# Kernel tuning notes

Hardware: AMD Instinct MI355X
Metric: run time of the kernel (lower is better)

## Reference

```python
import jax, jax.numpy as jnp
import numpy as np

E = 16           # num_experts
D = 4096         # hidden_size
F = 688          # per-expert SwiGLU intermediate size
N = 8192         # total tokens (bsz*seq_len)
CAP_FACTOR = 1.25


def setup_inputs() -> dict:
    key = jax.random.key(0)
    k1, k2, k3, k4, k5, k6 = jax.random.split(key, 6)
    return {
        "x": jax.random.normal(k1, (N, D), dtype=jnp.float32),
        "topk_idx": jax.random.randint(k2, (N,), 0, E, dtype=jnp.int32),
        "topk_scores": jax.random.uniform(k3, (N,), dtype=jnp.float32),
        "Wg": jax.random.normal(k4, (E, D, F), dtype=jnp.float32) * 0.02,
        "Wu": jax.random.normal(k5, (E, D, F), dtype=jnp.float32) * 0.02,
        "Wd": jax.random.normal(k6, (E, F, D), dtype=jnp.float32) * 0.02,
    }


def reference(x, topk_idx, topk_scores, Wg, Wu, Wd):
    # Switch-style top-1 MoE with capacity-based token dropping.
    # Deterministic variant: tokens beyond capacity are dropped in token order
    # (original uses randperm; the math pattern is identical).
    n, d = x.shape
    e = Wg.shape[0]
    cap = int(CAP_FACTOR * n / e)  # static under jit

    # position of each token within its assigned expert (0-based)
    oh = jax.nn.one_hot(topk_idx, e, dtype=jnp.int32)            # [N, E]
    pos = jnp.take_along_axis(jnp.cumsum(oh, axis=0) - 1,
                              topk_idx[:, None].astype(jnp.int32), axis=1)[:, 0]
    keep = pos < cap                                             # [N] bool

    # dispatch: scatter kept tokens into [E, cap, D]; dropped go to dummy row E
    e_safe = jnp.where(keep, topk_idx, e)
    p_safe = jnp.minimum(pos, cap - 1)
    buf = jnp.zeros((e + 1, cap, d), x.dtype).at[e_safe, p_safe].set(x)[:e]

    # per-expert SwiGLU FFN: down(silu(gate(x)) * up(x))
    h = jax.nn.silu(jnp.einsum('ecd,edf->ecf', buf, Wg)) \
        * jnp.einsum('ecd,edf->ecf', buf, Wu)                    # [E, cap, F]
    out = jnp.einsum('ecf,efd->ecd', h, Wd)                      # [E, cap, D]

    # combine: gather back, zero-pad dropped tokens, scale by gate scores
    y = out[topk_idx, p_safe] * keep[:, None].astype(x.dtype)
    y = y * topk_scores[:, None]
    return y
```

## Files before the change

### kernel.cpp

```cpp
#include <hip/hip_runtime.h>
#include <hip/hip_bf16.h>

#define E_ 16
#define D_ 4096
#define F_ 688
#define N_ 8192
#define CAP_ 640
#define NKT_ 64
#define NFT_ 11

typedef __attribute__((ext_vector_type(8))) short bf16x8;
typedef __attribute__((ext_vector_type(4))) float f32x4;
typedef __attribute__((ext_vector_type(4))) float fvec4;
typedef __attribute__((ext_vector_type(8))) unsigned short usvec8;

__device__ __forceinline__ unsigned short f2bf(float f) {
    __hip_bfloat16 h = __float2bfloat16(f);
    return __builtin_bit_cast(unsigned short, h);
}
__device__ __forceinline__ int lidx(int row, int k) {
    return row * 64 + (((k >> 3) ^ (row & 7)) << 3) + (k & 7);
}
__device__ __forceinline__ int bidx(int row, int k) {
    return row * 64 + (((k >> 3) ^ ((row >> 1) & 7)) << 3) + (k & 7);
}
__device__ __forceinline__ void gload16(const unsigned short* g, unsigned short* l) {
    __builtin_amdgcn_global_load_lds(
        (const __attribute__((address_space(1))) unsigned int*)g,
        (__attribute__((address_space(3))) unsigned int*)l, 16, 0, 0);
}

__global__ void k_dispatch(const int* __restrict__ idx,
                           int* __restrict__ slot_token,
                           int* __restrict__ row_of,
                           int* __restrict__ cnt) {
    __shared__ int hist[256][E_];
    const int t = threadIdx.x;
#pragma unroll
    for (int e = 0; e < E_; e++) hist[t][e] = 0;
    __syncthreads();
    const int base = t * (N_ / 256);
    for (int j = 0; j < N_ / 256; j++) {
        int e = idx[base + j];
        hist[t][e]++;
    }
    __syncthreads();
    if (t < E_) {
        int run = 0;
        for (int i = 0; i < 256; i++) { int v = hist[i][t]; hist[i][t] = run; run += v; }
        cnt[t] = run < CAP_ ? run : CAP_;
    }
    for (int s = t; s < E_ * CAP_; s += 256) slot_token[s] = -1;
    __syncthreads();
    for (int j = 0; j < N_ / 256; j++) {
        int i = base + j;
        int e = idx[i];
        int p = hist[t][e]++;
        if (p < CAP_) { slot_token[e * CAP_ + p] = i; row_of[i] = e * CAP_ + p; }
        else          { row_of[i] = -1; }
    }
}

__global__ void k_zero_dropped(const int* __restrict__ row_of, float* __restrict__ y) {
    const int i = blockIdx.x;
    if (row_of[i] >= 0) return;
    fvec4* yp = (fvec4*)(y + (size_t)i * D_);
    fvec4 z = {0.f, 0.f, 0.f, 0.f};
    for (int c = threadIdx.x; c < D_ / 4; c += 256) yp[c] = z;
}

__global__ void k_gather(const float* __restrict__ x, const int* __restrict__ slot_token,
                         unsigned short* __restrict__ Aimg) {
    const int strip = blockIdx.y;
    const int kg = blockIdx.x;
    const int t = threadIdx.x;
    const int r = t >> 1, h = t & 1;
    const int tok = slot_token[strip * 128 + r];
#pragma unroll
    for (int kl4 = 0; kl4 < 4; kl4++) {
        const int kt = kg * 4 + kl4;
        const int k0 = kt * 64 + h * 32;
        unsigned short* dst = Aimg + ((size_t)strip * NKT_ + kt) * 8192;
        usvec8 p[4];
        if (tok < 0) {
            usvec8 z = {0, 0, 0, 0, 0, 0, 0, 0};
            p[0] = z; p[1] = z; p[2] = z; p[3] = z;
        } else {
            const float* src = x + (size_t)tok * D_ + k0;
#pragma unroll
            for (int uu = 0; uu < 4; uu++) {
                fvec4 a = *(const fvec4*)(src + uu * 8);
                fvec4 b = *(const fvec4*)(src + uu * 8 + 4);
                usvec8 q = {f2bf(a[0]), f2bf(a[1]), f2bf(a[2]), f2bf(a[3]),
                            f2bf(b[0]), f2bf(b[1]), f2bf(b[2]), f2bf(b[3])};
                p[uu] = q;
            }
        }
#pragma unroll
        for (int uu = 0; uu < 4; uu++)
            *(usvec8*)&dst[lidx(r, h * 32 + uu * 8)] = p[uu];
    }
}

__global__ __launch_bounds__(256, 2) void k_gemm1(
    const unsigned short* __restrict__ Aimg,
    const float* __restrict__ Wg, const float* __restrict__ Wu,
    const int* __restrict__ cnt, unsigned short* __restrict__ Himg) {
    const int bid = blockIdx.x;
    const int xcd = bid & 7;
    const int j = bid >> 3;
    const int mb = j % 5;
    const int gl = j / 5;
    const int group = xcd * 22 + gl;
    const int e = group / NFT_, fidx = group % NFT_;
    const int m0 = mb * 128, f0 = fidx * 64;
    if (m0 >= cnt[e]) return;
    const int strip = e * 5 + mb;

    __shared__ __align__(16) unsigned short As[2][128 * 64];
    __shared__ __align__(16) unsigned short Bgs[2][64 * 64];
    __shared__ __align__(16) unsigned short Bus[2][64 * 64];

    const int tid = threadIdx.x;
    const int lane = tid & 63, wave = tid >> 6;
    const int wm = wave >> 1, wn = wave & 1;

    f32x4 accG[4][2], accU[4][2];
#pragma unroll
    for (int a = 0; a < 4; a++)
#pragma unroll
        for (int b = 0; b < 2; b++) {
            f32x4 z = {0.f, 0.f, 0.f, 0.f};
            accG[a][b] = z; accU[a][b] = z;
        }

    const int fpos = (tid & 31) * 2, kq8 = (tid >> 5) * 8;
    const int gf = f0 + fpos;
    const bool bvalid = gf < F_;
    const float2 fz2 = {0.f, 0.f};
    const float* WgE = Wg + (size_t)e * D_ * F_;
    const float* WuE = Wu + (size_t)e * D_ * F_;
    const unsigned short* Astrip = Aimg + (size_t)strip * NKT_ * 8192;

    {
#pragma unroll
        for (int i = 0; i < 4; i++) {
            int off = (wave * 4 + i) * 512;
            gload16(Astrip + off + lane * 8, &As[0][off]);
        }
        float2 g[8], u[8];
#pragma unroll
        for (int r = 0; r < 8; r++) {
            size_t off = (size_t)(kq8 + r) * F_ + gf;
            g[r] = bvalid ? *(const float2*)(WgE + off) : fz2;
            u[r] = bvalid ? *(const float2*)(WuE + off) : fz2;
        }
        usvec8 pg0, pg1, pu0, pu1;
#pragma unroll
        for (int r = 0; r < 8; r++) {
            pg0[r] = (short)f2bf(g[r].x); pg1[r] = (short)f2bf(g[r].y);
            pu0[r] = (short)f2bf(u[r].x); pu1[r] = (short)f2bf(u[r].y);
        }
        *(usvec8*)&Bgs[0][bidx(fpos, kq8)]     = pg0;
        *(usvec8*)&Bgs[0][bidx(fpos + 1, kq8)] = pg1;
        *(usvec8*)&Bus[0][bidx(fpos, kq8)]     = pu0;
        *(usvec8*)&Bus[0][bidx(fpos + 1, kq8)] = pu1;
    }
    __syncthreads();

    for (int kt = 0; kt < NKT_; ++kt) {
        const int cur = kt & 1, nxt = cur ^ 1;
        const bool hn = (kt + 1 < NKT_);
        float2 g[8], u[8];
        if (hn) {
            const unsigned short* asrc = Astrip + (size_t)(kt + 1) * 8192;
#pragma unroll
            for (int i = 0; i < 4; i++) {
                int off = (wave * 4 + i) * 512;
                gload16(asrc + off + lane * 8, &As[nxt][off]);
            }
#pragma unroll
            for (int r = 0; r < 8; r++) {
                size_t off = ((size_t)(kt + 1) * 64 + kq8 + r) * F_ + gf;
                g[r] = bvalid ? *(const float2*)(WgE + off) : fz2;
                u[r] = bvalid ? *(const float2*)(WuE + off) : fz2;
            }
        }
        __builtin_amdgcn_s_setprio(1);
#pragma unroll
        for (int kk = 0; kk < 64; kk += 32) {
            const int ko = kk + ((lane >> 4) << 3);
            bf16x8 av[4], bgv[2], buv[2];
#pragma unroll
            for (int mi = 0; mi < 4; mi++)
                av[mi] = *(const bf16x8*)&As[cur][lidx(wm * 64 + mi * 16 + (lane & 15), ko)];
#pragma unroll
            for (int ni = 0; ni < 2; ni++) {
                int rr = wn * 32 + ni * 16 + (lane & 15);
                bgv[ni] = *(const bf16x8*)&Bgs[cur][bidx(rr, ko)];
                buv[ni] = *(const bf16x8*)&Bus[cur][bidx(rr, ko)];
            }
#pragma unroll
            for (int mi = 0; mi < 4; mi++)
#pragma unroll
                for (int ni = 0; ni < 2; ni++) {
                    accG[mi][ni] = __builtin_amdgcn_mfma_f32_16x16x32_bf16(av[mi], bgv[ni], accG[mi][ni], 0, 0, 0);
                    accU[mi][ni] = __builtin_amdgcn_mfma_f32_16x16x32_bf16(av[mi], buv[ni], accU[mi][ni], 0, 0, 0);
                }
        }
        __builtin_amdgcn_s_setprio(0);
        if (hn) {
            usvec8 pg0, pg1, pu0, pu1;
#pragma unroll
            for (int r = 0; r < 8; r++) {
                pg0[r] = (short)f2bf(g[r].x); pg1[r] = (short)f2bf(g[r].y);
                pu0[r] = (short)f2bf(u[r].x); pu1[r] = (short)f2bf(u[r].y);
            }
            *(usvec8*)&Bgs[nxt][bidx(fpos, kq8)]     = pg0;
            *(usvec8*)&Bgs[nxt][bidx(fpos + 1, kq8)] = pg1;
            *(usvec8*)&Bus[nxt][bidx(fpos, kq8)]     = pu0;
            *(usvec8*)&Bus[nxt][bidx(fpos + 1, kq8)] = pu1;
        }
        __syncthreads();
    }

    unsigned short* Ht = Himg + ((size_t)strip * NFT_ + fidx) * 8192;
#pragma unroll
    for (int mi = 0; mi < 4; mi++)
#pragma unroll
        for (int ni = 0; ni < 2; ni++) {
            int fl = wn * 32 + ni * 16 + (lane & 15);
            int rl = wm * 64 + mi * 16 + ((lane >> 4) << 2);
#pragma unroll
            for (int q = 0; q < 4; q++) {
                float g = accG[mi][ni][q], u = accU[mi][ni][q];
                float h = g * u / (1.f + __expf(-g));
                Ht[lidx(rl + q, fl)] = f2bf(h);
            }
        }
}

__global__ __launch_bounds__(256, 3) void k_gemm2(
    const unsigned short* __restrict__ Himg, const float* __restrict__ Wd,
    const int* __restrict__ slot_token, const int* __restrict__ cnt,
    const float* __restrict__ scores, float* __restrict__ y) {
    const int bid = blockIdx.x;
    const int xcd = bid & 7;
    const int j = bid >> 3;
    const int mb = j % 5;
    const int gl = j / 5;
    const int group = xcd * 128 + gl;
    const int e = group >> 6, didx = group & 63;
    const int m0 = mb * 128, d0 = didx * 64;
    if (m0 >= cnt[e]) return;
    const int strip = e * 5 + mb;

    __shared__ __align__(16) unsigned short As[2][128 * 64];
    __shared__ __align__(16) unsigned short Bts[2][64 * 64];
    __shared__ int tokS[128];
    __shared__ float scS[128];

    const int tid = threadIdx.x;
    const int lane = tid & 63, wave = tid >> 6;
    const int wm = wave >> 1, wn = wave & 1;

    if (tid < 128) {
        int t = slot_token[e * CAP_ + m0 + tid];
        tokS[tid] = t;
        scS[tid] = (t >= 0) ? scores[t] : 0.f;
    }

    f32x4 acc[4][2];
#pragma unroll
    for (int a = 0; a < 4; a++)
#pragma unroll
        for (int b = 0; b < 2; b++) {
            f32x4 z = {0.f, 0.f, 0.f, 0.f};
            acc[a][b] = z;
        }

    const int dpos = (tid & 31) * 2, kq8 = (tid >> 5) * 8;
    const int gd = d0 + dpos;
    const float2 fz2 = {0.f, 0.f};
    const float* WdE = Wd + (size_t)e * F_ * D_;
    const unsigned short* Hstrip = Himg + (size_t)strip * NFT_ * 8192;

    {
#pragma unroll
        for (int i = 0; i < 4; i++) {
            int off = (wave * 4 + i) * 512;
            gload16(Hstrip + off + lane * 8, &As[0][off]);
        }
        float2 b[8];
#pragma unroll
        for (int r = 0; r < 8; r++) {
            int kr = kq8 + r;
            b[r] = (kr < F_) ? *(const float2*)(WdE + (size_t)kr * D_ + gd) : fz2;
        }
        usvec8 p0, p1;
#pragma unroll
        for (int r = 0; r < 8; r++) { p0[r] = (short)f2bf(b[r].x); p1[r] = (short)f2bf(b[r].y); }
        *(usvec8*)&Bts[0][bidx(dpos, kq8)]     = p0;
        *(usvec8*)&Bts[0][bidx(dpos + 1, kq8)] = p1;
    }
    __syncthreads();

    for (int fc = 0; fc < NFT_; ++fc) {
        const int cur = fc & 1, nxt = cur ^ 1;
        const bool hn = (fc + 1 < NFT_);
        float2 b[8];
        if (hn) {
            const unsigned short* asrc = Hstrip + (size_t)(fc + 1) * 8192;
#pragma unroll
            for (int i = 0; i < 4; i++) {
                int off = (wave * 4 + i) * 512;
                gload16(asrc + off + lane * 8, &As[nxt][off]);
            }
#pragma unroll
            for (int r = 0; r < 8; r++) {
                int kr = (fc + 1) * 64 + kq8 + r;
                b[r] = (kr < F_) ? *(const float2*)(WdE + (size_t)kr * D_ + gd) : fz2;
            }
        }
        __builtin_amdgcn_s_setprio(1);
#pragma unroll
        for (int kk = 0; kk < 64; kk += 32) {
            const int ko = kk + ((lane >> 4) << 3);
            bf16x8 av[4], bv[2];
#pragma unroll
            for (int mi = 0; mi < 4; mi++)
                av[mi] = *(const bf16x8*)&As[cur][lidx(wm * 64 + mi * 16 + (lane & 15), ko)];
#pragma unroll
            for (int ni = 0; ni < 2; ni++)
                bv[ni] = *(const bf16x8*)&Bts[cur][bidx(wn * 32 + ni * 16 + (lane & 15), ko)];
#pragma unroll
            for (int mi = 0; mi < 4; mi++)
#pragma unroll
                for (int ni = 0; ni < 2; ni++)
                    acc[mi][ni] = __builtin_amdgcn_mfma_f32_16x16x32_bf16(av[mi], bv[ni], acc[mi][ni], 0, 0, 0);
        }
        __builtin_amdgcn_s_setprio(0);
        if (hn) {
            usvec8 p0, p1;
#pragma unroll
            for (int r = 0; r < 8; r++) { p0[r] = (short)f2bf(b[r].x); p1[r] = (short)f2bf(b[r].y); }
            *(usvec8*)&Bts[nxt][bidx(dpos, kq8)]     = p0;
            *(usvec8*)&Bts[nxt][bidx(dpos + 1, kq8)] = p1;
        }
        __syncthreads();
    }

#pragma unroll
    for (int mi = 0; mi < 4; mi++)
#pragma unroll
        for (int ni = 0; ni < 2; ni++) {
            int d = d0 + wn * 32 + ni * 16 + (lane & 15);
            int rowb = wm * 64 + mi * 16 + ((lane >> 4) << 2);
#pragma unroll
            for (int q = 0; q < 4; q++) {
                int row = rowb + q;
                int t = tokS[row];
                if (t >= 0) y[(size_t)t * D_ + d] = acc[mi][ni][q] * scS[row];
            }
        }
}

extern "C" void kernel_launch(void* const* d_in, const int* in_sizes, int n_in,
                              void* d_out, int out_size, void* d_ws, size_t ws_size,
                              hipStream_t stream) {
    const float* x   = (const float*)d_in[0];
    const int*   idx = (const int*)d_in[1];
    const float* sc  = (const float*)d_in[2];
    const float* Wg  = (const float*)d_in[3];
    const float* Wu  = (const float*)d_in[4];
    const float* Wd  = (const float*)d_in[5];
    float* y = (float*)d_out;

    char* ws = (char*)d_ws;
    int* slot_token = (int*)ws;
    int* row_of     = (int*)(ws + 40960);
    int* cnt        = (int*)(ws + 40960 + 32768);
    const size_t hoff = 131072;
    const size_t hbytes = (size_t)80 * NFT_ * 8192 * 2;
    unsigned short* Himg = (unsigned short*)(ws + hoff);
    const size_t aoff = hoff + hbytes;
    unsigned short* Aimg = (unsigned short*)(ws + aoff);

    k_dispatch<<<1, 256, 0, stream>>>(idx, slot_token, row_of, cnt);
    k_zero_dropped<<<N_, 256, 0, stream>>>(row_of, y);
    k_gather<<<dim3(16, 80), 256, 0, stream>>>(x, slot_token, Aimg);
    k_gemm1<<<880, 256, 0, stream>>>(Aimg, Wg, Wu, cnt, Himg);
    k_gemm2<<<5120, 256, 0, stream>>>(Himg, Wd, slot_token, cnt, sc, y);
}
```

Before: 476.3 us.

## Triple-buffer A tiles with two-ahead async loads and explicit vmcnt waits

Both GEMM kernels now keep three LDS buffers for the activation tile and issue the direct-to-LDS loads two iterations ahead. __syncthreads is replaced by explicit s_waitcnt vmcnt/lgkmcnt plus s_barrier, with sched_barriers to stop the compiler reordering. The goal is to hide global-load latency on the A operand behind more MFMA work. In exchange it uses more LDS per block, and gemm2's launch bounds drop from 3 to 2 blocks per CU, which may lower occupancy. The hand-counted vmcnt values must match the number of loads actually in flight, or the kernel reads stale data.

```diff
diff --git a/kernel.cpp b/kernel.cpp
--- a/kernel.cpp
+++ b/kernel.cpp
@@ -101,6 +101,11 @@
             *(usvec8*)&dst[lidx(r, h * 32 + uu * 8)] = p[uu];
     }
 }
+
+#define WAITV(N) asm volatile("s_waitcnt vmcnt(" #N ")" ::: "memory")
+#define WAITL    asm volatile("s_waitcnt lgkmcnt(0)" ::: "memory")
+#define SBAR     __builtin_amdgcn_s_barrier()
+#define SCHED0   __builtin_amdgcn_sched_barrier(0)
 
 __global__ __launch_bounds__(256, 2) void k_gemm1(
     const unsigned short* __restrict__ Aimg,
@@ -117,7 +122,7 @@
     if (m0 >= cnt[e]) return;
     const int strip = e * 5 + mb;
 
-    __shared__ __align__(16) unsigned short As[2][128 * 64];
+    __shared__ __align__(16) unsigned short As[3][128 * 64];
     __shared__ __align__(16) unsigned short Bgs[2][64 * 64];
     __shared__ __align__(16) unsigned short Bus[2][64 * 64];
 
@@ -141,13 +146,9 @@
     const float* WgE = Wg + (size_t)e * D_ * F_;
     const float* WuE = Wu + (size_t)e * D_ * F_;
     const unsigned short* Astrip = Aimg + (size_t)strip * NKT_ * 8192;
+    const int aoff0 = wave * 4 * 512;
 
     {
-#pragma unroll
-        for (int i = 0; i < 4; i++) {
-            int off = (wave * 4 + i) * 512;
-            gload16(Astrip + off + lane * 8, &As[0][off]);
-        }
         float2 g[8], u[8];
 #pragma unroll
         for (int r = 0; r < 8; r++) {
@@ -155,6 +156,12 @@
             g[r] = bvalid ? *(const float2*)(WgE + off) : fz2;
             u[r] = bvalid ? *(const float2*)(WuE + off) : fz2;
         }
+#pragma unroll
+        for (int i = 0; i < 4; i++)
+            gload16(Astrip + aoff0 + i * 512 + lane * 8, &As[0][aoff0 + i * 512]);
+#pragma unroll
+        for (int i = 0; i < 4; i++)
+            gload16(Astrip + 8192 + aoff0 + i * 512 + lane * 8, &As[1][aoff0 + i * 512]);
         usvec8 pg0, pg1, pu0, pu1;
 #pragma unroll
         for (int r = 0; r < 8; r++) {
@@ -166,19 +173,16 @@
         *(usvec8*)&Bus[0][bidx(fpos, kq8)]     = pu0;
         *(usvec8*)&Bus[0][bidx(fpos + 1, kq8)] = pu1;
     }
-    __syncthreads();
+    WAITV(4);
+    WAITL;
+    SBAR;
+    SCHED0;
 
     for (int kt = 0; kt < NKT_; ++kt) {
-        const int cur = kt & 1, nxt = cur ^ 1;
-        const bool hn = (kt + 1 < NKT_);
+        const int cur3 = kt % 3, curb = kt & 1;
+        const bool hb = (kt + 1 < NKT_), ha = (kt + 2 < NKT_);
         float2 g[8], u[8];
-        if (hn) {
-            const unsigned short* asrc = Astrip + (size_t)(kt + 1) * 8192;
-#pragma unroll
-            for (int i = 0; i < 4; i++) {
-                int off = (wave * 4 + i) * 512;
-                gload16(asrc + off + lane * 8, &As[nxt][off]);
-            }
+        if (hb) {
 #pragma unroll
             for (int r = 0; r < 8; r++) {
                 size_t off = ((size_t)(kt + 1) * 64 + kq8 + r) * F_ + gf;
@@ -186,6 +190,14 @@
                 u[r] = bvalid ? *(const float2*)(WuE + off) : fz2;
             }
         }
+        if (ha) {
+            const unsigned short* asrc = Astrip + (size_t)(kt + 2) * 8192 + aoff0;
+            unsigned short* adst = &As[(kt + 2) % 3][aoff0];
+#pragma unroll
+            for (int i = 0; i < 4; i++)
+                gload16(asrc + i * 512 + lane * 8, adst + i * 512);
+        }
+        SCHED0;
         __builtin_amdgcn_s_setprio(1);
 #pragma unroll
         for (int kk = 0; kk < 64; kk += 32) {
@@ -193,12 +205,12 @@
             bf16x8 av[4], bgv[2], buv[2];
 #pragma unroll
             for (int mi = 0; mi < 4; mi++)
-                av[mi] = *(const bf16x8*)&As[cur][lidx(wm * 64 + mi * 16 + (lane & 15), ko)];
+                av[mi] = *(const bf16x8*)&As[cur3][lidx(wm * 64 + mi * 16 + (lane & 15), ko)];
 #pragma unroll
             for (int ni = 0; ni < 2; ni++) {
                 int rr = wn * 32 + ni * 16 + (lane & 15);
-                bgv[ni] = *(const bf16x8*)&Bgs[cur][bidx(rr, ko)];
-                buv[ni] = *(const bf16x8*)&Bus[cur][bidx(rr, ko)];
+                bgv[ni] = *(const bf16x8*)&Bgs[curb][bidx(rr, ko)];
+                buv[ni] = *(const bf16x8*)&Bus[curb][bidx(rr, ko)];
             }
 #pragma unroll
             for (int mi = 0; mi < 4; mi++)
@@ -209,19 +221,24 @@
                 }
         }
         __builtin_amdgcn_s_setprio(0);
-        if (hn) {
+        SCHED0;
+        if (hb) {
             usvec8 pg0, pg1, pu0, pu1;
 #pragma unroll
             for (int r = 0; r < 8; r++) {
                 pg0[r] = (short)f2bf(g[r].x); pg1[r] = (short)f2bf(g[r].y);
                 pu0[r] = (short)f2bf(u[r].x); pu1[r] = (short)f2bf(u[r].y);
             }
-            *(usvec8*)&Bgs[nxt][bidx(fpos, kq8)]     = pg0;
-            *(usvec8*)&Bgs[nxt][bidx(fpos + 1, kq8)] = pg1;
-            *(usvec8*)&Bus[nxt][bidx(fpos, kq8)]     = pu0;
-            *(usvec8*)&Bus[nxt][bidx(fpos + 1, kq8)] = pu1;
-        }
-        __syncthreads();
+            const int nb = curb ^ 1;
+            *(usvec8*)&Bgs[nb][bidx(fpos, kq8)]     = pg0;
+            *(usvec8*)&Bgs[nb][bidx(fpos + 1, kq8)] = pg1;
+            *(usvec8*)&Bus[nb][bidx(fpos, kq8)]     = pu0;
+            *(usvec8*)&Bus[nb][bidx(fpos + 1, kq8)] = pu1;
+        }
+        if (ha) WAITV(4); else WAITV(0);
+        WAITL;
+        SBAR;
+        SCHED0;
     }
 
     unsigned short* Ht = Himg + ((size_t)strip * NFT_ + fidx) * 8192;
@@ -240,7 +257,7 @@
         }
 }
 
-__global__ __launch_bounds__(256, 3) void k_gemm2(
+__global__ __launch_bounds__(256, 2) void k_gemm2(
     const unsigned short* __restrict__ Himg, const float* __restrict__ Wd,
     const int* __restrict__ slot_token, const int* __restrict__ cnt,
     const float* __restrict__ scores, float* __restrict__ y) {
@@ -255,7 +272,7 @@
     if (m0 >= cnt[e]) return;
     const int strip = e * 5 + mb;
 
-    __shared__ __align__(16) unsigned short As[2][128 * 64];
+    __shared__ __align__(16) unsigned short As[3][128 * 64];
     __shared__ __align__(16) unsigned short Bts[2][64 * 64];
     __shared__ int tokS[128];
     __shared__ float scS[128];
@@ -284,44 +301,51 @@
     const float2 fz2 = {0.f, 0.f};
     const float* WdE = Wd + (size_t)e * F_ * D_;
     const unsigned short* Hstrip = Himg + (size_t)strip * NFT_ * 8192;
+    const int aoff0 = wave * 4 * 512;
 
     {
-#pragma unroll
-        for (int i = 0; i < 4; i++) {
-            int off = (wave * 4 + i) * 512;
-            gload16(Hstrip + off + lane * 8, &As[0][off]);
-        }
         float2 b[8];
 #pragma unroll
         for (int r = 0; r < 8; r++) {
             int kr = kq8 + r;
             b[r] = (kr < F_) ? *(const float2*)(WdE + (size_t)kr * D_ + gd) : fz2;
         }
+#pragma unroll
+        for (int i = 0; i < 4; i++)
+            gload16(Hstrip + aoff0 + i * 512 + lane * 8, &As[0][aoff0 + i * 512]);
+#pragma unroll
+        for (int i = 0; i < 4; i++)
+            gload16(Hstrip + 8192 + aoff0 + i * 512 + lane * 8, &As[1][aoff0 + i * 512]);
         usvec8 p0, p1;
 #pragma unroll
         for (int r = 0; r < 8; r++) { p0[r] = (short)f2bf(b[r].x); p1[r] = (short)f2bf(b[r].y); }
         *(usvec8*)&Bts[0][bidx(dpos, kq8)]     = p0;
         *(usvec8*)&Bts[0][bidx(dpos + 1, kq8)] = p1;
     }
-    __syncthreads();
+    WAITV(4);
+    WAITL;
+    SBAR;
+    SCHED0;
 
     for (int fc = 0; fc < NFT_; ++fc) {
-        const int cur = fc & 1, nxt = cur ^ 1;
-        const bool hn = (fc + 1 < NFT_);
+        const int cur3 = fc % 3, curb = fc & 1;
+        const bool hb = (fc + 1 < NFT_), ha = (fc + 2 < NFT_);
         float2 b[8];
-        if (hn) {
-            const unsigned short* asrc = Hstrip + (size_t)(fc + 1) * 8192;
-#pragma unroll
-            for (int i = 0; i < 4; i++) {
-                int off = (wave * 4 + i) * 512;
-                gload16(asrc + off + lane * 8, &As[nxt][off]);
-            }
+        if (hb) {
 #pragma unroll
             for (int r = 0; r < 8; r++) {
                 int kr = (fc + 1) * 64 + kq8 + r;
                 b[r] = (kr < F_) ? *(const float2*)(WdE + (size_t)kr * D_ + gd) : fz2;
             }
         }
+        if (ha) {
+            const unsigned short* asrc = Hstrip + (size_t)(fc + 2) * 8192 + aoff0;
+            unsigned short* adst = &As[(fc + 2) % 3][aoff0];
+#pragma unroll
+            for (int i = 0; i < 4; i++)
+                gload16(asrc + i * 512 + lane * 8, adst + i * 512);
+        }
+        SCHED0;
         __builtin_amdgcn_s_setprio(1);
 #pragma unroll
         for (int kk = 0; kk < 64; kk += 32) {
@@ -329,10 +353,10 @@
             bf16x8 av[4], bv[2];
 #pragma unroll
             for (int mi = 0; mi < 4; mi++)
-                av[mi] = *(const bf16x8*)&As[cur][lidx(wm * 64 + mi * 16 + (lane & 15), ko)];
+                av[mi] = *(const bf16x8*)&As[cur3][lidx(wm * 64 + mi * 16 + (lane & 15), ko)];
 #pragma unroll
             for (int ni = 0; ni < 2; ni++)
-                bv[ni] = *(const bf16x8*)&Bts[cur][bidx(wn * 32 + ni * 16 + (lane & 15), ko)];
+                bv[ni] = *(const bf16x8*)&Bts[curb][bidx(wn * 32 + ni * 16 + (lane & 15), ko)];
 #pragma unroll
             for (int mi = 0; mi < 4; mi++)
 #pragma unroll
@@ -340,14 +364,19 @@
                     acc[mi][ni] = __builtin_amdgcn_mfma_f32_16x16x32_bf16(av[mi], bv[ni], acc[mi][ni], 0, 0, 0);
         }
         __builtin_amdgcn_s_setprio(0);
-        if (hn) {
+        SCHED0;
+        if (hb) {
             usvec8 p0, p1;
 #pragma unroll
             for (int r = 0; r < 8; r++) { p0[r] = (short)f2bf(b[r].x); p1[r] = (short)f2bf(b[r].y); }
-            *(usvec8*)&Bts[nxt][bidx(dpos, kq8)]     = p0;
-            *(usvec8*)&Bts[nxt][bidx(dpos + 1, kq8)] = p1;
-        }
-        __syncthreads();
+            const int nb = curb ^ 1;
+            *(usvec8*)&Bts[nb][bidx(dpos, kq8)]     = p0;
+            *(usvec8*)&Bts[nb][bidx(dpos + 1, kq8)] = p1;
+        }
+        if (ha) WAITV(4); else WAITV(0);
+        WAITL;
+        SBAR;
+        SCHED0;
     }
 
 #pragma unroll
```

New measurement: 520.9 us. 1.09x slower.

## Pre-convert weights to bf16 swizzled images and stream tiles via LDS DMA

Applied to the files above, without the earlier changes.

Adds two prep kernels that convert Wg/Wu and Wd from fp32 into bf16 tile images in the already-swizzled LDS layout. The GEMM kernels then load the B tiles with direct global-to-LDS loads through a triple-buffered pipeline with explicit vmcnt waits, instead of doing register loads, conversion and LDS stores in the main loop. This removes per-block conversion work and register pressure from the GEMMs. The cost is an extra full pass over all weights each call, plus extra workspace.

```diff
diff --git a/kernel.cpp b/kernel.cpp
--- a/kernel.cpp
+++ b/kernel.cpp
@@ -29,6 +29,10 @@
         (const __attribute__((address_space(1))) unsigned int*)g,
         (__attribute__((address_space(3))) unsigned int*)l, 16, 0, 0);
 }
+
+#define WAITV(N) asm volatile("s_waitcnt vmcnt(" #N ")" ::: "memory")
+#define SBAR     __builtin_amdgcn_s_barrier()
+#define SCHED0   __builtin_amdgcn_sched_barrier(0)
 
 __global__ void k_dispatch(const int* __restrict__ idx,
                            int* __restrict__ slot_token,
@@ -102,9 +106,56 @@
     }
 }
 
-__global__ __launch_bounds__(256, 2) void k_gemm1(
-    const unsigned short* __restrict__ Aimg,
-    const float* __restrict__ Wg, const float* __restrict__ Wu,
+__global__ void k_wprep_gu(const float* __restrict__ Wg, const float* __restrict__ Wu,
+                           unsigned short* __restrict__ img) {
+    const int ft = blockIdx.x, kt = blockIdx.y, e = blockIdx.z;
+    const int tid = threadIdx.x;
+    const int fpos = (tid & 31) * 2, kq8 = (tid >> 5) * 8;
+    const int gf = ft * 64 + fpos;
+    const bool v = gf < F_;
+    const float2 fz2 = {0.f, 0.f};
+    float2 g[8], u[8];
+#pragma unroll
+    for (int r = 0; r < 8; r++) {
+        size_t off = (size_t)e * D_ * F_ + (size_t)(kt * 64 + kq8 + r) * F_ + gf;
+        g[r] = v ? *(const float2*)(Wg + off) : fz2;
+        u[r] = v ? *(const float2*)(Wu + off) : fz2;
+    }
+    usvec8 pg0, pg1, pu0, pu1;
+#pragma unroll
+    for (int r = 0; r < 8; r++) {
+        pg0[r] = (short)f2bf(g[r].x); pg1[r] = (short)f2bf(g[r].y);
+        pu0[r] = (short)f2bf(u[r].x); pu1[r] = (short)f2bf(u[r].y);
+    }
+    unsigned short* t = img + ((size_t)(e * NKT_ + kt) * NFT_ + ft) * 8192;
+    *(usvec8*)&t[bidx(fpos, kq8)]            = pg0;
+    *(usvec8*)&t[bidx(fpos + 1, kq8)]        = pg1;
+    *(usvec8*)&t[4096 + bidx(fpos, kq8)]     = pu0;
+    *(usvec8*)&t[4096 + bidx(fpos + 1, kq8)] = pu1;
+}
+
+__global__ void k_wprep_d(const float* __restrict__ Wd, unsigned short* __restrict__ img) {
+    const int dt = blockIdx.x, kt = blockIdx.y, e = blockIdx.z;
+    const int tid = threadIdx.x;
+    const int dpos = (tid & 31) * 2, kq8 = (tid >> 5) * 8;
+    const int gd = dt * 64 + dpos;
+    const float2 fz2 = {0.f, 0.f};
+    float2 b[8];
+#pragma unroll
+    for (int r = 0; r < 8; r++) {
+        int krow = kt * 64 + kq8 + r;
+        b[r] = (krow < F_) ? *(const float2*)(Wd + (size_t)e * F_ * D_ + (size_t)krow * D_ + gd) : fz2;
+    }
+    usvec8 p0, p1;
+#pragma unroll
+    for (int r = 0; r < 8; r++) { p0[r] = (short)f2bf(b[r].x); p1[r] = (short)f2bf(b[r].y); }
+    unsigned short* t = img + ((size_t)(e * NFT_ + kt) * 64 + dt) * 4096;
+    *(usvec8*)&t[bidx(dpos, kq8)]     = p0;
+    *(usvec8*)&t[bidx(dpos + 1, kq8)] = p1;
+}
+
+__global__ __launch_bounds__(256, 2) void k_gemm1_dma(
+    const unsigned short* __restrict__ Aimg, const unsigned short* __restrict__ Wgu,
     const int* __restrict__ cnt, unsigned short* __restrict__ Himg) {
     const int bid = blockIdx.x;
     const int xcd = bid & 7;
@@ -113,17 +164,18 @@
     const int gl = j / 5;
     const int group = xcd * 22 + gl;
     const int e = group / NFT_, fidx = group % NFT_;
-    const int m0 = mb * 128, f0 = fidx * 64;
+    const int m0 = mb * 128;
     if (m0 >= cnt[e]) return;
     const int strip = e * 5 + mb;
 
-    __shared__ __align__(16) unsigned short As[2][128 * 64];
-    __shared__ __align__(16) unsigned short Bgs[2][64 * 64];
-    __shared__ __align__(16) unsigned short Bus[2][64 * 64];
+    __shared__ __align__(16) unsigned short As[2][8192];
+    __shared__ __align__(16) unsigned short Bgs[3][4096];
+    __shared__ __align__(16) unsigned short Bus[3][4096];
 
     const int tid = threadIdx.x;
     const int lane = tid & 63, wave = tid >> 6;
     const int wm = wave >> 1, wn = wave & 1;
+    const int aw4 = wave * 4, bw2 = wave * 2;
 
     f32x4 accG[4][2], accU[4][2];
 #pragma unroll
@@ -134,58 +186,35 @@
             accG[a][b] = z; accU[a][b] = z;
         }
 
-    const int fpos = (tid & 31) * 2, kq8 = (tid >> 5) * 8;
-    const int gf = f0 + fpos;
-    const bool bvalid = gf < F_;
-    const float2 fz2 = {0.f, 0.f};
-    const float* WgE = Wg + (size_t)e * D_ * F_;
-    const float* WuE = Wu + (size_t)e * D_ * F_;
     const unsigned short* Astrip = Aimg + (size_t)strip * NKT_ * 8192;
-
-    {
-#pragma unroll
-        for (int i = 0; i < 4; i++) {
-            int off = (wave * 4 + i) * 512;
-            gload16(Astrip + off + lane * 8, &As[0][off]);
-        }
-        float2 g[8], u[8];
-#pragma unroll
-        for (int r = 0; r < 8; r++) {
-            size_t off = (size_t)(kq8 + r) * F_ + gf;
-            g[r] = bvalid ? *(const float2*)(WgE + off) : fz2;
-            u[r] = bvalid ? *(const float2*)(WuE + off) : fz2;
-        }
-        usvec8 pg0, pg1, pu0, pu1;
-#pragma unroll
-        for (int r = 0; r < 8; r++) {
-            pg0[r] = (short)f2bf(g[r].x); pg1[r] = (short)f2bf(g[r].y);
-            pu0[r] = (short)f2bf(u[r].x); pu1[r] = (short)f2bf(u[r].y);
-        }
-        *(usvec8*)&Bgs[0][bidx(fpos, kq8)]     = pg0;
-        *(usvec8*)&Bgs[0][bidx(fpos + 1, kq8)] = pg1;
-        *(usvec8*)&Bus[0][bidx(fpos, kq8)]     = pu0;
-        *(usvec8*)&Bus[0][bidx(fpos + 1, kq8)] = pu1;
-    }
-    __syncthreads();
+    const unsigned short* WguE = Wgu + (size_t)e * NKT_ * NFT_ * 8192 + (size_t)fidx * 8192;
+
+#define G1_A(T, BUF)                                                           \
+    {                                                                          \
+        const unsigned short* asrc = Astrip + (size_t)(T) * 8192;              \
+        _Pragma("unroll") for (int i = 0; i < 4; i++)                          \
+            gload16(asrc + (aw4 + i) * 512 + lane * 8, &As[BUF][(aw4 + i) * 512]); \
+    }
+#define G1_B(T, BUF)                                                           \
+    {                                                                          \
+        const unsigned short* bsrc = WguE + (size_t)(T) * (NFT_ * 8192);       \
+        _Pragma("unroll") for (int i = 0; i < 2; i++)                          \
+            gload16(bsrc + (bw2 + i) * 512 + lane * 8, &Bgs[BUF][(bw2 + i) * 512]); \
+        _Pragma("unroll") for (int i = 0; i < 2; i++)                          \
+            gload16(bsrc + 4096 + (bw2 + i) * 512 + lane * 8, &Bus[BUF][(bw2 + i) * 512]); \
+    }
+
+    G1_A(0, 0)
+    G1_B(0, 0)
+    G1_B(1, 1)
+    WAITV(4);
+    SBAR;
 
     for (int kt = 0; kt < NKT_; ++kt) {
-        const int cur = kt & 1, nxt = cur ^ 1;
-        const bool hn = (kt + 1 < NKT_);
-        float2 g[8], u[8];
-        if (hn) {
-            const unsigned short* asrc = Astrip + (size_t)(kt + 1) * 8192;
-#pragma unroll
-            for (int i = 0; i < 4; i++) {
-                int off = (wave * 4 + i) * 512;
-                gload16(asrc + off + lane * 8, &As[nxt][off]);
-            }
-#pragma unroll
-            for (int r = 0; r < 8; r++) {
-                size_t off = ((size_t)(kt + 1) * 64 + kq8 + r) * F_ + gf;
-                g[r] = bvalid ? *(const float2*)(WgE + off) : fz2;
-                u[r] = bvalid ? *(const float2*)(WuE + off) : fz2;
-            }
-        }
+        const int curA = kt & 1, curB = kt % 3;
+        if (kt + 1 < NKT_) G1_A(kt + 1, (kt + 1) & 1)
+        if (kt + 2 < NKT_) G1_B(kt + 2, (kt + 2) % 3)
+        SCHED0;
         __builtin_amdgcn_s_setprio(1);
 #pragma unroll
         for (int kk = 0; kk < 64; kk += 32) {
@@ -193,12 +222,12 @@
             bf16x8 av[4], bgv[2], buv[2];
 #pragma unroll
             for (int mi = 0; mi < 4; mi++)
-                av[mi] = *(const bf16x8*)&As[cur][lidx(wm * 64 + mi * 16 + (lane & 15), ko)];
+                av[mi] = *(const bf16x8*)&As[curA][lidx(wm * 64 + mi * 16 + (lane & 15), ko)];
 #pragma unroll
             for (int ni = 0; ni < 2; ni++) {
                 int rr = wn * 32 + ni * 16 + (lane & 15);
-                bgv[ni] = *(const bf16x8*)&Bgs[cur][bidx(rr, ko)];
-                buv[ni] = *(const bf16x8*)&Bus[cur][bidx(rr, ko)];
+                bgv[ni] = *(const bf16x8*)&Bgs[curB][bidx(rr, ko)];
+                buv[ni] = *(const bf16x8*)&Bus[curB][bidx(rr, ko)];
             }
 #pragma unroll
             for (int mi = 0; mi < 4; mi++)
@@ -209,20 +238,12 @@
                 }
         }
         __builtin_amdgcn_s_setprio(0);
-        if (hn) {
-            usvec8 pg0, pg1, pu0, pu1;
-#pragma unroll
-            for (int r = 0; r < 8; r++) {
-                pg0[r] = (short)f2bf(g[r].x); pg1[r] = (short)f2bf(g[r].y);
-                pu0[r] = (short)f2bf(u[r].x); pu1[r] = (short)f2bf(u[r].y);
-            }
-            *(usvec8*)&Bgs[nxt][bidx(fpos, kq8)]     = pg0;
-            *(usvec8*)&Bgs[nxt][bidx(fpos + 1, kq8)] = pg1;
-            *(usvec8*)&Bus[nxt][bidx(fpos, kq8)]     = pu0;
-            *(usvec8*)&Bus[nxt][bidx(fpos + 1, kq8)] = pu1;
-        }
-        __syncthreads();
-    }
+        SCHED0;
+        if (kt + 2 < NKT_) WAITV(4); else WAITV(0);
+        if (kt + 1 < NKT_) SBAR;
+    }
+#undef G1_A
+#undef G1_B
 
     unsigned short* Ht = Himg + ((size_t)strip * NFT_ + fidx) * 8192;
 #pragma unroll
@@ -240,8 +261,8 @@
         }
 }
 
-__global__ __launch_bounds__(256, 3) void k_gemm2(
-    const unsigned short* __restrict__ Himg, const float* __restrict__ Wd,
+__global__ __launch_bounds__(256, 2) void k_gemm2_dma(
+    const unsigned short* __restrict__ Himg, const unsigned short* __restrict__ WdI,
     const int* __restrict__ slot_token, const int* __restrict__ cnt,
     const float* __restrict__ scores, float* __restrict__ y) {
     const int bid = blockIdx.x;
@@ -255,20 +276,22 @@
     if (m0 >= cnt[e]) return;
     const int strip = e * 5 + mb;
 
-    __shared__ __align__(16) unsigned short As[2][128 * 64];
-    __shared__ __align__(16) unsigned short Bts[2][64 * 64];
+    __shared__ __align__(16) unsigned short As[2][8192];
+    __shared__ __align__(16) unsigned short Bts[3][4096];
     __shared__ int tokS[128];
     __shared__ float scS[128];
 
     const int tid = threadIdx.x;
     const int lane = tid & 63, wave = tid >> 6;
     const int wm = wave >> 1, wn = wave & 1;
+    const int aw4 = wave * 4, bw2 = wave * 2;
 
     if (tid < 128) {
         int t = slot_token[e * CAP_ + m0 + tid];
         tokS[tid] = t;
         scS[tid] = (t >= 0) ? scores[t] : 0.f;
     }
+    __syncthreads();
 
     f32x4 acc[4][2];
 #pragma unroll
@@ -279,49 +302,33 @@
             acc[a][b] = z;
         }
 
-    const int dpos = (tid & 31) * 2, kq8 = (tid >> 5) * 8;
-    const int gd = d0 + dpos;
-    const float2 fz2 = {0.f, 0.f};
-    const float* WdE = Wd + (size_t)e * F_ * D_;
     const unsigned short* Hstrip = Himg + (size_t)strip * NFT_ * 8192;
-
-    {
-#pragma unroll
-        for (int i = 0; i < 4; i++) {
-            int off = (wave * 4 + i) * 512;
-            gload16(Hstrip + off + lane * 8, &As[0][off]);
-        }
-        float2 b[8];
-#pragma unroll
-        for (int r = 0; r < 8; r++) {
-            int kr = kq8 + r;
-            b[r] = (kr < F_) ? *(const float2*)(WdE + (size_t)kr * D_ + gd) : fz2;
-        }
-        usvec8 p0, p1;
-#pragma unroll
-        for (int r = 0; r < 8; r++) { p0[r] = (short)f2bf(b[r].x); p1[r] = (short)f2bf(b[r].y); }
-        *(usvec8*)&Bts[0][bidx(dpos, kq8)]     = p0;
-        *(usvec8*)&Bts[0][bidx(dpos + 1, kq8)] = p1;
-    }
-    __syncthreads();
+    const unsigned short* WdE = WdI + (size_t)e * NFT_ * 64 * 4096 + (size_t)didx * 4096;
+
+#define G2_A(T, BUF)                                                           \
+    {                                                                          \
+        const unsigned short* asrc = Hstrip + (size_t)(T) * 8192;              \
+        _Pragma("unroll") for (int i = 0; i < 4; i++)                          \
+            gload16(asrc + (aw4 + i) * 512 + lane * 8, &As[BUF][(aw4 + i) * 512]); \
+    }
+#define G2_B(T, BUF)                                                           \
+    {                                                                          \
+        const unsigned short* bsrc = WdE + (size_t)(T) * (64 * 4096);          \
+        _Pragma("unroll") for (int i = 0; i < 2; i++)                          \
+            gload16(bsrc + (bw2 + i) * 512 + lane * 8, &Bts[BUF][(bw2 + i) * 512]); \
+    }
+
+    G2_A(0, 0)
+    G2_B(0, 0)
+    G2_B(1, 1)
+    WAITV(2);
+    SBAR;
 
     for (int fc = 0; fc < NFT_; ++fc) {
-        const int cur = fc & 1, nxt = cur ^ 1;
-        const bool hn = (fc + 1 < NFT_);
-        float2 b[8];
-        if (hn) {
-            const unsigned short* asrc = Hstrip + (size_t)(fc + 1) * 8192;
-#pragma unroll
-            for (int i = 0; i < 4; i++) {
-                int off = (wave * 4 + i) * 512;
-                gload16(asrc + off + lane * 8, &As[nxt][off]);
-            }
-#pragma unroll
-            for (int r = 0; r < 8; r++) {
-                int kr = (fc + 1) * 64 + kq8 + r;
-                b[r] = (kr < F_) ? *(const float2*)(WdE + (size_t)kr * D_ + gd) : fz2;
-            }
-        }
+        const int curA = fc & 1, curB = fc % 3;
+        if (fc + 1 < NFT_) G2_A(fc + 1, (fc + 1) & 1)
+        if (fc + 2 < NFT_) G2_B(fc + 2, (fc + 2) % 3)
+        SCHED0;
         __builtin_amdgcn_s_setprio(1);
 #pragma unroll
         for (int kk = 0; kk < 64; kk += 32) {
@@ -329,10 +336,10 @@
             bf16x8 av[4], bv[2];
 #pragma unroll
             for (int mi = 0; mi < 4; mi++)
-                av[mi] = *(const bf16x8*)&As[cur][lidx(wm * 64 + mi * 16 + (lane & 15), ko)];
+                av[mi] = *(const bf16x8*)&As[curA][lidx(wm * 64 + mi * 16 + (lane & 15), ko)];
 #pragma unroll
             for (int ni = 0; ni < 2; ni++)
-                bv[ni] = *(const bf16x8*)&Bts[cur][bidx(wn * 32 + ni * 16 + (lane & 15), ko)];
+                bv[ni] = *(const bf16x8*)&Bts[curB][bidx(wn * 32 + ni * 16 + (lane & 15), ko)];
 #pragma unroll
             for (int mi = 0; mi < 4; mi++)
 #pragma unroll
@@ -340,15 +347,12 @@
                     acc[mi][ni] = __builtin_amdgcn_mfma_f32_16x16x32_bf16(av[mi], bv[ni], acc[mi][ni], 0, 0, 0);
         }
         __builtin_amdgcn_s_setprio(0);
-        if (hn) {
-            usvec8 p0, p1;
-#pragma unroll
-            for (int r = 0; r < 8; r++) { p0[r] = (short)f2bf(b[r].x); p1[r] = (short)f2bf(b[r].y); }
-            *(usvec8*)&Bts[nxt][bidx(dpos, kq8)]     = p0;
-            *(usvec8*)&Bts[nxt][bidx(dpos + 1, kq8)] = p1;
-        }
-        __syncthreads();
-    }
+        SCHED0;
+        if (fc + 2 < NFT_) WAITV(2); else WAITV(0);
+        if (fc + 1 < NFT_) SBAR;
+    }
+#undef G2_A
+#undef G2_B
 
 #pragma unroll
     for (int mi = 0; mi < 4; mi++)
@@ -380,15 +384,23 @@
     int* slot_token = (int*)ws;
     int* row_of     = (int*)(ws + 40960);
     int* cnt        = (int*)(ws + 40960 + 32768);
-    const size_t hoff = 131072;
-    const size_t hbytes = (size_t)80 * NFT_ * 8192 * 2;
+    const size_t hoff   = 131072;
+    const size_t hbytes = (size_t)80 * NFT_ * 16384;
     unsigned short* Himg = (unsigned short*)(ws + hoff);
-    const size_t aoff = hoff + hbytes;
+    const size_t aoff   = hoff + hbytes;
+    const size_t abytes = (size_t)80 * NKT_ * 16384;
     unsigned short* Aimg = (unsigned short*)(ws + aoff);
+    const size_t guoff   = aoff + abytes;
+    const size_t gubytes = (size_t)E_ * NKT_ * NFT_ * 16384;
+    unsigned short* WguI = (unsigned short*)(ws + guoff);
+    const size_t wdoff   = guoff + gubytes;
+    unsigned short* WdI  = (unsigned short*)(ws + wdoff);
 
     k_dispatch<<<1, 256, 0, stream>>>(idx, slot_token, row_of, cnt);
     k_zero_dropped<<<N_, 256, 0, stream>>>(row_of, y);
     k_gather<<<dim3(16, 80), 256, 0, stream>>>(x, slot_token, Aimg);
-    k_gemm1<<<880, 256, 0, stream>>>(Aimg, Wg, Wu, cnt, Himg);
-    k_gemm2<<<5120, 256, 0, stream>>>(Himg, Wd, slot_token, cnt, sc, y);
-}
+    k_wprep_gu<<<dim3(NFT_, NKT_, E_), 256, 0, stream>>>(Wg, Wu, WguI);
+    k_wprep_d<<<dim3(64, NFT_, E_), 256, 0, stream>>>(Wd, WdI);
+    k_gemm1_dma<<<880, 256, 0, stream>>>(Aimg, WguI, cnt, Himg);
+    k_gemm2_dma<<<5120, 256, 0, stream>>>(Himg, WdI, slot_token, cnt, sc, y);
+}
```

Measured after the change: 554.1 us. +16.3%, slower.
